# Performance work log

Measured on AMD Instinct MI355X. Metric: run time of the kernel, lower is better.

Reference implementation:

```python
import jax, jax.numpy as jnp
import numpy as np
from jax import lax

B, L, D, N, R, NC = 8, 1024, 1024, 16, 64, 1000  # batch, seq, d_inner, d_state, dt_rank, num_classes


def setup_inputs() -> dict:
    key = jax.random.key(0)
    ks = jax.random.split(key, 6)
    x = jax.random.normal(ks[0], (B, L, D), dtype=jnp.float32)
    # Mamba S4D-real init: A = 1..N broadcast over channels, stored as log
    A_log = jnp.log(jnp.broadcast_to(jnp.arange(1, N + 1, dtype=jnp.float32), (D, N)))
    D_param = jnp.ones((D,), dtype=jnp.float32)
    W_xproj = jax.random.normal(ks[1], (R + 2 * N, D), dtype=jnp.float32) * 0.02
    W_dt = jax.random.normal(ks[2], (D, R), dtype=jnp.float32) * 0.02
    b_dt = jax.random.normal(ks[3], (D,), dtype=jnp.float32) * 0.02
    W_cls = jax.random.normal(ks[4], (NC, D), dtype=jnp.float32) * 0.02
    b_cls = jnp.zeros((NC,), dtype=jnp.float32)
    return {"x": x, "A_log": A_log, "D_param": D_param, "W_xproj": W_xproj,
            "W_dt": W_dt, "b_dt": b_dt, "W_cls": W_cls, "b_cls": b_cls}


def reference(x, A_log, D_param, W_xproj, W_dt, b_dt, W_cls, b_cls):
    # x: [B, L, D] -> project to dt_rank + 2*d_state (no bias, as in Mamba)
    xdb = jnp.einsum('bld,kd->blk', x, W_xproj)          # [B, L, R+2N]
    dt_r = xdb[..., :R]                                   # [B, L, R]
    Bm = xdb[..., R:R + N]                                # [B, L, N]
    Cm = xdb[..., R + N:]                                 # [B, L, N]
    # softplus on dt
    dt = jax.nn.softplus(jnp.einsum('blr,dr->bld', dt_r, W_dt) + b_dt)  # [B, L, D]
    # discretization
    A = -jnp.exp(A_log)                                   # [D, N]
    dA = jnp.exp(dt[..., None] * A)                       # [B, L, D, N]
    dBx = dt[..., None] * Bm[:, :, None, :] * x[..., None]  # [B, L, D, N]

    # sequential scan over time
    def step(h, inp):
        dA_t, dBx_t, C_t = inp                            # [B,D,N],[B,D,N],[B,N]
        h = dA_t * h + dBx_t
        y = jnp.einsum('bdn,bn->bd', h, C_t)
        return h, y

    h0 = jnp.zeros((B, D, N), dtype=x.dtype)
    _, ys = lax.scan(step, h0, (jnp.moveaxis(dA, 1, 0),
                                jnp.moveaxis(dBx, 1, 0),
                                jnp.moveaxis(Cm, 1, 0)))   # ys: [L, B, D]
    y = jnp.moveaxis(ys, 0, 1) + D_param * x              # [B, L, D] skip term

    pooled = y.mean(axis=1)                               # AdaptiveAvgPool1d(1) over L
    logits = pooled @ W_cls.T + b_cls                     # [B, NC]
    return logits
```

## Files before the change

### kernel.cpp

```cpp
#include <hip/hip_runtime.h>
#include <hip/hip_bf16.h>

#define B_  8
#define L_  1024
#define D_  1024
#define N_  16
#define R_  64
#define NC_ 1000

#define XP_KS   8
#define XP_TM   64
#define XP_KC   (D_ / XP_KS)
#define XP_M    (B_ * L_)

#define CH8  8
#define TCH8 (L_ / CH8)
#define TB   32

__device__ __forceinline__ float exp2_fast(float a) {
#if __has_builtin(__builtin_amdgcn_exp2f)
  return __builtin_amdgcn_exp2f(a);
#else
  float r;
  asm("v_exp_f32 %0, %1" : "=v"(r) : "v"(a));
  return r;
#endif
}

__global__ __launch_bounds__(256) void xproj_kernel(
    const float* __restrict__ x, const float* __restrict__ W,
    float* __restrict__ part) {
  __shared__ float xs[XP_TM][36];
  __shared__ float wt[32][100];
  const int tid = threadIdx.x;
  const int tx = tid & 7;
  const int ty = tid >> 3;
  const int m0 = blockIdx.x * XP_TM;
  const int ks = blockIdx.y;

  float acc[2][12];
#pragma unroll
  for (int r = 0; r < 2; ++r)
#pragma unroll
    for (int j = 0; j < 12; ++j) acc[r][j] = 0.f;

  for (int step = 0; step < XP_KC / 32; ++step) {
    const int kbase = ks * XP_KC + step * 32;
    __syncthreads();
#pragma unroll
    for (int j = 0; j < 2; ++j) {
      const int f4 = tid + j * 256;
      const int row = f4 >> 3, c4 = f4 & 7;
      float4 v = *(const float4*)(x + (size_t)(m0 + row) * D_ + kbase + c4 * 4);
      *(float4*)(&xs[row][c4 * 4]) = v;
    }
#pragma unroll
    for (int j = 0; j < 3; ++j) {
      const int idx = tid + j * 256;
      const int wr = idx >> 3, c4 = idx & 7;
      float4 v = *(const float4*)(W + (size_t)wr * D_ + kbase + c4 * 4);
      wt[c4 * 4 + 0][wr] = v.x;
      wt[c4 * 4 + 1][wr] = v.y;
      wt[c4 * 4 + 2][wr] = v.z;
      wt[c4 * 4 + 3][wr] = v.w;
    }
    __syncthreads();
#pragma unroll 4
    for (int kk = 0; kk < 32; ++kk) {
      const float a0 = xs[ty * 2 + 0][kk];
      const float a1 = xs[ty * 2 + 1][kk];
      const float4 b0 = *(const float4*)(&wt[kk][tx * 12 + 0]);
      const float4 b1 = *(const float4*)(&wt[kk][tx * 12 + 4]);
      const float4 b2 = *(const float4*)(&wt[kk][tx * 12 + 8]);
      acc[0][0] = fmaf(a0, b0.x, acc[0][0]);
      acc[0][1] = fmaf(a0, b0.y, acc[0][1]);
      acc[0][2] = fmaf(a0, b0.z, acc[0][2]);
      acc[0][3] = fmaf(a0, b0.w, acc[0][3]);
      acc[0][4] = fmaf(a0, b1.x, acc[0][4]);
      acc[0][5] = fmaf(a0, b1.y, acc[0][5]);
      acc[0][6] = fmaf(a0, b1.z, acc[0][6]);
      acc[0][7] = fmaf(a0, b1.w, acc[0][7]);
      acc[0][8] = fmaf(a0, b2.x, acc[0][8]);
      acc[0][9] = fmaf(a0, b2.y, acc[0][9]);
      acc[0][10] = fmaf(a0, b2.z, acc[0][10]);
      acc[0][11] = fmaf(a0, b2.w, acc[0][11]);
      acc[1][0] = fmaf(a1, b0.x, acc[1][0]);
      acc[1][1] = fmaf(a1, b0.y, acc[1][1]);
      acc[1][2] = fmaf(a1, b0.z, acc[1][2]);
      acc[1][3] = fmaf(a1, b0.w, acc[1][3]);
      acc[1][4] = fmaf(a1, b1.x, acc[1][4]);
      acc[1][5] = fmaf(a1, b1.y, acc[1][5]);
      acc[1][6] = fmaf(a1, b1.z, acc[1][6]);
      acc[1][7] = fmaf(a1, b1.w, acc[1][7]);
      acc[1][8] = fmaf(a1, b2.x, acc[1][8]);
      acc[1][9] = fmaf(a1, b2.y, acc[1][9]);
      acc[1][10] = fmaf(a1, b2.z, acc[1][10]);
      acc[1][11] = fmaf(a1, b2.w, acc[1][11]);
    }
  }
#pragma unroll
  for (int r = 0; r < 2; ++r) {
    float* p = part + ((size_t)ks * XP_M + m0 + ty * 2 + r) * 96 + tx * 12;
    *(float4*)(p + 0) = make_float4(acc[r][0], acc[r][1], acc[r][2], acc[r][3]);
    *(float4*)(p + 4) = make_float4(acc[r][4], acc[r][5], acc[r][6], acc[r][7]);
    *(float4*)(p + 8) = make_float4(acc[r][8], acc[r][9], acc[r][10], acc[r][11]);
  }
}

__global__ __launch_bounds__(256) void xreduce_kernel(
    const float* __restrict__ part, float* __restrict__ xdb) {
  const size_t gidx = (size_t)blockIdx.x * 256 + threadIdx.x;
  const float4* p4 = (const float4*)part;
  const size_t stride = (size_t)XP_M * 96 / 4;
  float4 s = p4[gidx];
#pragma unroll
  for (int ks = 1; ks < XP_KS; ++ks) {
    const float4 v = p4[(size_t)ks * stride + gidx];
    s.x += v.x; s.y += v.y; s.z += v.z; s.w += v.w;
  }
  ((float4*)xdb)[gidx] = s;
}

__global__ __launch_bounds__(256) void dt_kernel(
    const float* __restrict__ xdb, const float* __restrict__ W_dt,
    const float* __restrict__ b_dt, float* __restrict__ dtb) {
  __shared__ float xst[64][68];
  __shared__ float wt[64][68];
  const int tid = threadIdx.x;
  const int tx = tid & 15;
  const int ty = tid >> 4;
  const int m0 = blockIdx.x * 64;
  const int d0 = blockIdx.y * 64;

  {
    const int qc = tid & 15, rr = tid >> 4;
#pragma unroll
    for (int j = 0; j < 4; ++j) {
      const int row = rr + j * 16;
      const float4 a = *(const float4*)(xdb + (size_t)(m0 + row) * 96 + qc * 4);
      xst[qc * 4 + 0][row] = a.x;
      xst[qc * 4 + 1][row] = a.y;
      xst[qc * 4 + 2][row] = a.z;
      xst[qc * 4 + 3][row] = a.w;
      const float4 w = *(const float4*)(W_dt + (size_t)(d0 + row) * R_ + qc * 4);
      wt[qc * 4 + 0][row] = w.x;
      wt[qc * 4 + 1][row] = w.y;
      wt[qc * 4 + 2][row] = w.z;
      wt[qc * 4 + 3][row] = w.w;
    }
  }
  __syncthreads();

  float acc[4][4];
#pragma unroll
  for (int i = 0; i < 4; ++i)
#pragma unroll
    for (int j = 0; j < 4; ++j) acc[i][j] = 0.f;

#pragma unroll
  for (int k = 0; k < 64; ++k) {
    const float4 bq = *(const float4*)(&wt[k][tx * 4]);
    const float4 aq = *(const float4*)(&xst[k][ty * 4]);
#pragma unroll
    for (int mi = 0; mi < 4; ++mi) {
      const float a = (mi == 0) ? aq.x : (mi == 1) ? aq.y : (mi == 2) ? aq.z : aq.w;
      acc[mi][0] = fmaf(a, bq.x, acc[mi][0]);
      acc[mi][1] = fmaf(a, bq.y, acc[mi][1]);
      acc[mi][2] = fmaf(a, bq.z, acc[mi][2]);
      acc[mi][3] = fmaf(a, bq.w, acc[mi][3]);
    }
  }

  const float4 bd = *(const float4*)(b_dt + d0 + tx * 4);
#pragma unroll
  for (int mi = 0; mi < 4; ++mi) {
    float4 o;
    float s;
    s = acc[mi][0] + bd.x;
    o.x = fmaxf(s, 0.f) + __logf(1.0f + __expf(-fabsf(s)));
    s = acc[mi][1] + bd.y;
    o.y = fmaxf(s, 0.f) + __logf(1.0f + __expf(-fabsf(s)));
    s = acc[mi][2] + bd.z;
    o.z = fmaxf(s, 0.f) + __logf(1.0f + __expf(-fabsf(s)));
    s = acc[mi][3] + bd.w;
    o.w = fmaxf(s, 0.f) + __logf(1.0f + __expf(-fabsf(s)));
    *(float4*)(dtb + (size_t)(m0 + ty * 4 + mi) * D_ + d0 + tx * 4) = o;
  }
}

__global__ __launch_bounds__(256) void scan_kernel(
    const float* __restrict__ x, const float* __restrict__ xdb,
    const float* __restrict__ dtb, const float* __restrict__ A_log,
    float* __restrict__ summ, float* __restrict__ sumx) {
  __shared__ float dts[TB][32];
  __shared__ float dtx[TB][32];
  __shared__ float bcs[TB][34];
  const int tid = threadIdx.x;
  const int n = tid & 15;
  const int dl = tid >> 4;
  const int b = blockIdx.x >> 5;
  const int dtile = blockIdx.x & 31;
  const int c = blockIdx.y;
  const int d0 = dtile * 32;
  const int da = d0 + 2 * dl, db = da + 1;

  const float Av0 = -__expf(A_log[(size_t)da * N_ + n]) * 1.44269504089f;
  const float Av1 = -__expf(A_log[(size_t)db * N_ + n]) * 1.44269504089f;

  const int t0 = c * TCH8;
  float cumP0 = 1.f, loc0 = 0.f, S10 = 0.f, S20 = 0.f;
  float cumP1 = 1.f, loc1 = 0.f, S11 = 0.f, S21 = 0.f;
  float xp0 = 0.f, xp1 = 0.f, xp2 = 0.f, xp3 = 0.f;

  const int srow = tid >> 3, sc4 = (tid & 7) * 4;
  const int bpos = ((sc4 * 2) & 31) + (sc4 >> 4);

  for (int tb = 0; tb < TCH8; tb += TB) {
    const int tbase = t0 + tb;
    __syncthreads();
    {
      const size_t g = ((size_t)b * L_ + tbase + srow) * D_ + d0 + sc4;
      const float4 xv = *(const float4*)(x + g);
      const float4 dv = *(const float4*)(dtb + g);
      *(float4*)(&dts[srow][sc4]) = dv;
      *(float4*)(&dtx[srow][sc4]) =
          make_float4(xv.x * dv.x, xv.y * dv.y, xv.z * dv.z, xv.w * dv.w);
      xp0 += xv.x; xp1 += xv.y; xp2 += xv.z; xp3 += xv.w;
      const size_t gb = ((size_t)b * L_ + tbase + srow) * 96 + 64 + sc4;
      const float4 bc = *(const float4*)(xdb + gb);
      bcs[srow][bpos + 0] = bc.x;
      bcs[srow][bpos + 2] = bc.y;
      bcs[srow][bpos + 4] = bc.z;
      bcs[srow][bpos + 6] = bc.w;
    }
    __syncthreads();
#pragma unroll
    for (int tt = 0; tt < TB; ++tt) {
      const float2 bv = *(const float2*)(&bcs[tt][2 * n]);
      const float2 dv = *(const float2*)(&dts[tt][2 * dl]);
      const float2 px = *(const float2*)(&dtx[tt][2 * dl]);
      const float e0 = exp2_fast(dv.x * Av0);
      cumP0 *= e0;
      loc0 = fmaf(e0, loc0, px.x * bv.x);
      S10 = fmaf(cumP0, bv.y, S10);
      S20 = fmaf(loc0, bv.y, S20);
      const float e1 = exp2_fast(dv.y * Av1);
      cumP1 *= e1;
      loc1 = fmaf(e1, loc1, px.y * bv.x);
      S11 = fmaf(cumP1, bv.y, S11);
      S21 = fmaf(loc1, bv.y, S21);
    }
  }
  const size_t si0 = (((size_t)c * B_ + b) * D_ + da) * N_ + n;
  const size_t si1 = (((size_t)c * B_ + b) * D_ + db) * N_ + n;
  ((float4*)summ)[si0] = make_float4(cumP0, S10, S20, loc0);
  ((float4*)summ)[si1] = make_float4(cumP1, S11, S21, loc1);

  __syncthreads();
  *(float4*)(&dtx[srow][sc4]) = make_float4(xp0, xp1, xp2, xp3);
  __syncthreads();
  if (tid < 32) {
    float s = 0.f;
#pragma unroll
    for (int r = 0; r < 32; ++r) s += dtx[r][tid];
    sumx[((size_t)c * B_ + b) * D_ + d0 + tid] = s;
  }
}

__global__ __launch_bounds__(256) void combine_kernel(
    const float* __restrict__ summ, const float* __restrict__ sumx,
    const float* __restrict__ D_param, float* __restrict__ pooled) {
  const int gid = blockIdx.x * 256 + threadIdx.x;
  const int n = gid & 15;
  const int d = (gid >> 4) & (D_ - 1);
  const int b = gid >> 14;
  float hin = 0.f, acc = 0.f;
  const float4* s4 = (const float4*)summ;
#pragma unroll
  for (int c = 0; c < CH8; ++c) {
    const float4 f = s4[(((size_t)c * B_ + b) * D_ + d) * N_ + n];
    acc = fmaf(hin, f.y, acc) + f.z;
    hin = fmaf(f.x, hin, f.w);
  }
  acc += __shfl_xor(acc, 1);
  acc += __shfl_xor(acc, 2);
  acc += __shfl_xor(acc, 4);
  acc += __shfl_xor(acc, 8);
  if (n == 0) {
    float xst = 0.f;
#pragma unroll
    for (int c = 0; c < CH8; ++c)
      xst += sumx[((size_t)c * B_ + b) * D_ + d];
    pooled[(size_t)b * D_ + d] =
        (acc + D_param[d] * xst) * (1.0f / (float)L_);
  }
}

__global__ __launch_bounds__(256) void cls_kernel(
    const float* __restrict__ pooled, const float* __restrict__ W_cls,
    const float* __restrict__ b_cls, float* __restrict__ out) {
  __shared__ float pool[B_ * D_];
  const int tid = threadIdx.x;
  const int c = blockIdx.x * 4 + (tid >> 6);
  const int lane = tid & 63;

#pragma unroll
  for (int j = 0; j < 8; ++j) {
    const int f4 = tid + j * 256;
    ((float4*)pool)[f4] = ((const float4*)pooled)[f4];
  }
  __syncthreads();

  float accb[B_];
#pragma unroll
  for (int b = 0; b < B_; ++b) accb[b] = 0.f;

#pragma unroll
  for (int i = 0; i < 4; ++i) {
    const float4 wv =
        *(const float4*)(W_cls + (size_t)c * D_ + i * 256 + lane * 4);
#pragma unroll
    for (int b = 0; b < B_; ++b) {
      const float4 p = *(const float4*)(&pool[b * D_ + i * 256 + lane * 4]);
      accb[b] = fmaf(wv.x, p.x,
                fmaf(wv.y, p.y, fmaf(wv.z, p.z, fmaf(wv.w, p.w, accb[b]))));
    }
  }
#pragma unroll
  for (int off = 1; off < 64; off <<= 1) {
#pragma unroll
    for (int b = 0; b < B_; ++b) accb[b] += __shfl_xor(accb[b], off);
  }
  if (lane < B_) out[(size_t)lane * NC_ + c] = accb[lane] + b_cls[c];
}

extern "C" void kernel_launch(void* const* d_in, const int* in_sizes, int n_in,
                              void* d_out, int out_size, void* d_ws,
                              size_t ws_size, hipStream_t stream) {
  const float* x = (const float*)d_in[0];
  const float* A_log = (const float*)d_in[1];
  const float* D_param = (const float*)d_in[2];
  const float* W_xproj = (const float*)d_in[3];
  const float* W_dt = (const float*)d_in[4];
  const float* b_dt = (const float*)d_in[5];
  const float* W_cls = (const float*)d_in[6];
  const float* b_cls = (const float*)d_in[7];
  float* out = (float*)d_out;

  float* ws_f = (float*)d_ws;
  float* xdb = ws_f;
  float* part = xdb + (size_t)XP_M * 96;
  float* dtb = part + (size_t)XP_KS * XP_M * 96;
  float* summ = dtb + (size_t)XP_M * D_;
  float* sumx = summ + (size_t)CH8 * B_ * D_ * N_ * 4;
  float* pooled = sumx + (size_t)CH8 * B_ * D_;

  xproj_kernel<<<dim3(XP_M / XP_TM, XP_KS), dim3(256), 0, stream>>>(
      x, W_xproj, part);
  xreduce_kernel<<<dim3(XP_M * 96 / 4 / 256), dim3(256), 0, stream>>>(part,
                                                                      xdb);
  dt_kernel<<<dim3(XP_M / 64, D_ / 64), dim3(256), 0, stream>>>(xdb, W_dt,
                                                                b_dt, dtb);
  scan_kernel<<<dim3(B_ * 32, CH8), dim3(256), 0, stream>>>(x, xdb, dtb,
                                                            A_log, summ, sumx);
  combine_kernel<<<dim3(B_ * D_ * N_ / 256), dim3(256), 0, stream>>>(
      summ, sumx, D_param, pooled);
  cls_kernel<<<dim3(NC_ / 4), dim3(256), 0, stream>>>(pooled, W_cls, b_cls,
                                                      out);
}
```

Measured before the change: 103.1 us.

## Read x and dt directly from global in scan, stage only B/C in LDS

The scan kernel no longer stages x and dt tiles through shared memory in 32-step blocks. It loads the whole chunk's B/C values into LDS once, then each thread streams its own float2 of x and dt straight from global memory per timestep. The thread mapping is swapped so the d index varies fastest within a wavefront, which makes those global reads coalesced across 16 lanes, and the per-chunk x sum is now kept in registers. This removes the per-block syncthreads and LDS round-trips, but each x/dt element is now read by 16 threads (one per state index), which relies on cache hits and lengthens the dependency on global load latency.

```diff
diff --git a/kernel.cpp b/kernel.cpp
--- a/kernel.cpp
+++ b/kernel.cpp
@@ -15,7 +15,6 @@
 
 #define CH8  8
 #define TCH8 (L_ / CH8)
-#define TB   32
 
 __device__ __forceinline__ float exp2_fast(float a) {
 #if __has_builtin(__builtin_amdgcn_exp2f)
@@ -192,78 +191,65 @@
     const float* __restrict__ x, const float* __restrict__ xdb,
     const float* __restrict__ dtb, const float* __restrict__ A_log,
     float* __restrict__ summ, float* __restrict__ sumx) {
-  __shared__ float dts[TB][32];
-  __shared__ float dtx[TB][32];
-  __shared__ float bcs[TB][34];
+  __shared__ float bcs[TCH8][34];
   const int tid = threadIdx.x;
-  const int n = tid & 15;
-  const int dl = tid >> 4;
+  const int dl = tid & 15;
+  const int n = tid >> 4;
   const int b = blockIdx.x >> 5;
   const int dtile = blockIdx.x & 31;
   const int c = blockIdx.y;
   const int d0 = dtile * 32;
-  const int da = d0 + 2 * dl, db = da + 1;
-
-  const float Av0 = -__expf(A_log[(size_t)da * N_ + n]) * 1.44269504089f;
-  const float Av1 = -__expf(A_log[(size_t)db * N_ + n]) * 1.44269504089f;
-
+  const int da = d0 + 2 * dl;
   const int t0 = c * TCH8;
-  float cumP0 = 1.f, loc0 = 0.f, S10 = 0.f, S20 = 0.f;
-  float cumP1 = 1.f, loc1 = 0.f, S11 = 0.f, S21 = 0.f;
-  float xp0 = 0.f, xp1 = 0.f, xp2 = 0.f, xp3 = 0.f;
-
-  const int srow = tid >> 3, sc4 = (tid & 7) * 4;
-  const int bpos = ((sc4 * 2) & 31) + (sc4 >> 4);
-
-  for (int tb = 0; tb < TCH8; tb += TB) {
-    const int tbase = t0 + tb;
-    __syncthreads();
-    {
-      const size_t g = ((size_t)b * L_ + tbase + srow) * D_ + d0 + sc4;
-      const float4 xv = *(const float4*)(x + g);
-      const float4 dv = *(const float4*)(dtb + g);
-      *(float4*)(&dts[srow][sc4]) = dv;
-      *(float4*)(&dtx[srow][sc4]) =
-          make_float4(xv.x * dv.x, xv.y * dv.y, xv.z * dv.z, xv.w * dv.w);
-      xp0 += xv.x; xp1 += xv.y; xp2 += xv.z; xp3 += xv.w;
-      const size_t gb = ((size_t)b * L_ + tbase + srow) * 96 + 64 + sc4;
-      const float4 bc = *(const float4*)(xdb + gb);
-      bcs[srow][bpos + 0] = bc.x;
-      bcs[srow][bpos + 2] = bc.y;
-      bcs[srow][bpos + 4] = bc.z;
-      bcs[srow][bpos + 6] = bc.w;
-    }
-    __syncthreads();
-#pragma unroll
-    for (int tt = 0; tt < TB; ++tt) {
-      const float2 bv = *(const float2*)(&bcs[tt][2 * n]);
-      const float2 dv = *(const float2*)(&dts[tt][2 * dl]);
-      const float2 px = *(const float2*)(&dtx[tt][2 * dl]);
-      const float e0 = exp2_fast(dv.x * Av0);
-      cumP0 *= e0;
-      loc0 = fmaf(e0, loc0, px.x * bv.x);
-      S10 = fmaf(cumP0, bv.y, S10);
-      S20 = fmaf(loc0, bv.y, S20);
-      const float e1 = exp2_fast(dv.y * Av1);
-      cumP1 *= e1;
-      loc1 = fmaf(e1, loc1, px.y * bv.x);
-      S11 = fmaf(cumP1, bv.y, S11);
-      S21 = fmaf(loc1, bv.y, S21);
-    }
-  }
-  const size_t si0 = (((size_t)c * B_ + b) * D_ + da) * N_ + n;
-  const size_t si1 = (((size_t)c * B_ + b) * D_ + db) * N_ + n;
-  ((float4*)summ)[si0] = make_float4(cumP0, S10, S20, loc0);
-  ((float4*)summ)[si1] = make_float4(cumP1, S11, S21, loc1);
-
+
+#pragma unroll
+  for (int j = 0; j < 4; ++j) {
+    const int f4 = tid + j * 256;
+    const int row = f4 >> 3;
+    const int bc4 = (f4 & 7) * 4;
+    const float4 v =
+        *(const float4*)(xdb + ((size_t)b * L_ + t0 + row) * 96 + 64 + bc4);
+    const int bpos = ((bc4 * 2) & 31) + (bc4 >> 4);
+    bcs[row][bpos + 0] = v.x;
+    bcs[row][bpos + 2] = v.y;
+    bcs[row][bpos + 4] = v.z;
+    bcs[row][bpos + 6] = v.w;
+  }
+  const float LOG2E = 1.44269504089f;
+  const float Av0 = -__expf(A_log[(size_t)da * N_ + n]) * LOG2E;
+  const float Av1 = -__expf(A_log[(size_t)(da + 1) * N_ + n]) * LOG2E;
   __syncthreads();
-  *(float4*)(&dtx[srow][sc4]) = make_float4(xp0, xp1, xp2, xp3);
-  __syncthreads();
-  if (tid < 32) {
-    float s = 0.f;
-#pragma unroll
-    for (int r = 0; r < 32; ++r) s += dtx[r][tid];
-    sumx[((size_t)c * B_ + b) * D_ + d0 + tid] = s;
+
+  const float* xp = x + ((size_t)b * L_ + t0) * D_ + da;
+  const float* dp = dtb + ((size_t)b * L_ + t0) * D_ + da;
+
+  float cumP0 = 1.f, loc0 = 0.f, S10 = 0.f, S20 = 0.f, xs0 = 0.f;
+  float cumP1 = 1.f, loc1 = 0.f, S11 = 0.f, S21 = 0.f, xs1 = 0.f;
+
+#pragma unroll 4
+  for (int t = 0; t < TCH8; ++t) {
+    const float2 xv = *(const float2*)(xp + (size_t)t * D_);
+    const float2 dv = *(const float2*)(dp + (size_t)t * D_);
+    const float2 bc = *(const float2*)(&bcs[t][2 * n]);
+    const float e0 = exp2_fast(dv.x * Av0);
+    const float e1 = exp2_fast(dv.y * Av1);
+    cumP0 *= e0;
+    loc0 = fmaf(e0, loc0, (dv.x * xv.x) * bc.x);
+    S10 = fmaf(cumP0, bc.y, S10);
+    S20 = fmaf(loc0, bc.y, S20);
+    xs0 += xv.x;
+    cumP1 *= e1;
+    loc1 = fmaf(e1, loc1, (dv.y * xv.y) * bc.x);
+    S11 = fmaf(cumP1, bc.y, S11);
+    S21 = fmaf(loc1, bc.y, S21);
+    xs1 += xv.y;
+  }
+
+  const size_t si = (((size_t)c * B_ + b) * D_ + da) * N_ + n;
+  ((float4*)summ)[si] = make_float4(cumP0, S10, S20, loc0);
+  ((float4*)summ)[si + N_] = make_float4(cumP1, S11, S21, loc1);
+  if (n == 0) {
+    *(float2*)(&sumx[((size_t)c * B_ + b) * D_ + da]) = make_float2(xs0, xs1);
   }
 }
 
```

After: 136.3 us. +32.2%, slower.
